# Kernel optimization log

Measured on AMD Instinct MI355X. Metric: run time of the kernel, lower is better.

Reference implementation:

```python
import jax, jax.numpy as jnp
import numpy as np

N_NODES = 50000
N_EDGES = 3200000
FEAT_IN = 2048  # pools 2:1 down to 1024


def _gcn_conv(x, row, col, W, b, n):
    # PyG GCNConv: add self-loops, symmetric D^-1/2 (A+I) D^-1/2 normalization,
    # aggregate at target (col), then bias.
    xw = x @ W  # [n, out]
    ones = jnp.ones(row.shape[0], dtype=xw.dtype)
    deg = jax.ops.segment_sum(ones, col, num_segments=n)  # includes self-loops
    dis = jax.lax.rsqrt(deg)  # deg >= 1 because of self-loops
    norm = dis[row] * dis[col]  # [E+n]
    out = jax.ops.segment_sum(norm[:, None] * xw[row], col, num_segments=n)
    return out + b


def setup_inputs() -> dict:
    key = jax.random.key(0)
    ks = jax.random.split(key, 12)
    x = jax.random.normal(ks[0], (N_NODES, FEAT_IN), dtype=jnp.float32)
    edge_index = jax.random.randint(ks[1], (2, N_EDGES), 0, N_NODES, dtype=jnp.int64)
    def lin(k, fan_in, fan_out):
        s = 1.0 / np.sqrt(fan_in)
        kw, kb = jax.random.split(k)
        W = jax.random.uniform(kw, (fan_in, fan_out), jnp.float32, -s, s)
        b = jax.random.uniform(kb, (fan_out,), jnp.float32, -s, s)
        return W, b
    w0, b0 = lin(ks[2], 1024, 512)
    w1, b1 = lin(ks[3], 512, 128)
    w2, b2 = lin(ks[4], 128, 64)
    g1_w, g1_b = lin(ks[5], 64, 32)
    g2_w, g2_b = lin(ks[6], 32, 16)
    return {
        "x": x, "edge_index": edge_index,
        "ln_w": jnp.ones((1024,), jnp.float32), "ln_b": jnp.zeros((1024,), jnp.float32),
        "w0": w0, "b0": b0, "w1": w1, "b1": b1, "w2": w2, "b2": b2,
        "g1_w": g1_w, "g1_b": g1_b, "g2_w": g2_w, "g2_b": g2_b,
    }


def reference(x, edge_index, ln_w, ln_b, w0, b0, w1, b1, w2, b2, g1_w, g1_b, g2_w, g2_b):
    n = x.shape[0]
    # AdaptiveMaxPool1d(1024): L=2048 -> exact windows of 2, stride 2
    h = x.reshape(n, 1024, 2).max(axis=-1)
    # LayerNorm(1024)
    mu = h.mean(axis=-1, keepdims=True)
    var = jnp.mean((h - mu) ** 2, axis=-1, keepdims=True)
    h = (h - mu) * jax.lax.rsqrt(var + 1e-5) * ln_w + ln_b
    # MLP with ELU (dropout is identity in eval mode)
    h = jax.nn.elu(h @ w0 + b0)
    h = jax.nn.elu(h @ w1 + b1)
    h = jax.nn.elu(h @ w2 + b2)
    # edge_index with self-loops appended (constant structure)
    sl = jnp.arange(n, dtype=edge_index.dtype)
    row = jnp.concatenate([edge_index[0], sl])
    col = jnp.concatenate([edge_index[1], sl])
    h = jax.nn.elu(_gcn_conv(h, row, col, g1_w, g1_b, n))
    return _gcn_conv(h, row, col, g2_w, g2_b, n)
```

## Files before the change

kernel.cpp:

```cpp
#include <hip/hip_runtime.h>
#include <hip/hip_bf16.h>

#define N_NODES 50000
#define N_EDGES 3200000
#define NB1 196
#define NBLK1 782
#define CAP 20480

typedef __bf16 v8bf __attribute__((ext_vector_type(8)));
typedef __bf16 v2bf __attribute__((ext_vector_type(2)));
typedef float v4f __attribute__((ext_vector_type(4)));

__device__ __forceinline__ float elu_f(float x) { return x > 0.f ? x : (expf(x) - 1.f); }

__device__ __forceinline__ float4 bf4f(ushort4 u) {
    float4 r;
    r.x = __uint_as_float(((unsigned)u.x) << 16);
    r.y = __uint_as_float(((unsigned)u.y) << 16);
    r.z = __uint_as_float(((unsigned)u.z) << 16);
    r.w = __uint_as_float(((unsigned)u.w) << 16);
    return r;
}

#define GL16(gp, lp) __builtin_amdgcn_global_load_lds( \
    (const __attribute__((address_space(1))) void*)(gp), \
    (__attribute__((address_space(3))) void*)(lp), 16, 0, 0)

__global__ void pool_ln_kernel(const float* __restrict__ x,
                               const float* __restrict__ ln_w,
                               const float* __restrict__ ln_b,
                               __bf16* __restrict__ h0,
                               const float* __restrict__ w0, const float* __restrict__ w1,
                               const float* __restrict__ w2,
                               __bf16* __restrict__ w0t, __bf16* __restrict__ w1t,
                               __bf16* __restrict__ w2t, int* __restrict__ fill196) {
    int t = threadIdx.x;
    if (blockIdx.x < 2336) {
        int idx = blockIdx.x * 256 + t;
        if (idx < NB1) fill196[idx] = idx * CAP;
        if (idx < 524288) {
            int k = idx >> 9, n = idx & 511;
            w0t[(size_t)n * 1024 + k] = (__bf16)w0[idx];
        } else if (idx < 524288 + 65536) {
            int j = idx - 524288;
            int k = j >> 7, n = j & 127;
            w1t[(size_t)n * 512 + k] = (__bf16)w1[j];
        } else if (idx < 524288 + 65536 + 8192) {
            int j = idx - 524288 - 65536;
            int k = j >> 6, n = j & 63;
            w2t[(size_t)n * 128 + k] = (__bf16)w2[j];
        }
    }
    int wave = t >> 6, lane = t & 63;
    int node = blockIdx.x * 4 + wave;
    const float4* xr = (const float4*)(x + (size_t)node * 2048);
    float4 v[8];
    #pragma unroll
    for (int j = 0; j < 8; ++j) v[j] = xr[j * 64 + lane];
    float p[16];
    float sum = 0.f, sq = 0.f;
    #pragma unroll
    for (int j = 0; j < 8; ++j) {
        p[2 * j]     = fmaxf(v[j].x, v[j].y);
        p[2 * j + 1] = fmaxf(v[j].z, v[j].w);
        sum += p[2 * j] + p[2 * j + 1];
        sq  += p[2 * j] * p[2 * j] + p[2 * j + 1] * p[2 * j + 1];
    }
    #pragma unroll
    for (int off = 32; off > 0; off >>= 1) {
        sum += __shfl_xor(sum, off);
        sq  += __shfl_xor(sq, off);
    }
    float mu = sum * (1.f / 1024.f);
    float var = sq * (1.f / 1024.f) - mu * mu;
    float rstd = rsqrtf(var + 1e-5f);
    const float2* w2p = (const float2*)ln_w;
    const float2* b2p = (const float2*)ln_b;
    #pragma unroll
    for (int j = 0; j < 8; ++j) {
        int c2 = j * 64 + lane;
        float2 w = w2p[c2], b = b2p[c2];
        v2bf o;
        o[0] = (__bf16)((p[2 * j]     - mu) * rstd * w.x + b.x);
        o[1] = (__bf16)((p[2 * j + 1] - mu) * rstd * w.y + b.y);
        *(v2bf*)(h0 + (size_t)node * 1024 + 2 * c2) = o;
    }
}

__global__ __launch_bounds__(512) void mfma_gemm0(
    const __bf16* __restrict__ A, const __bf16* __restrict__ BT,
    const float* __restrict__ bias, __bf16* __restrict__ C, int M)
{
    const int K = 1024, N = 512;
    __shared__ unsigned short lds[12288];
    const int tid = threadIdx.x;
    const int lane = tid & 63, w = tid >> 6;
    const int wr = w >> 2, wc = w & 3;
    const int m0 = blockIdx.x * 128, n0 = blockIdx.y * 256;

    int grA = m0 + (tid >> 2); if (grA > M - 1) grA = M - 1;
    const __bf16* aP = A + (size_t)grA * K + (tid & 3) * 8;
    char* ldsA = (char*)lds + tid * 16;
    const __bf16* bP0 = BT + (size_t)(n0 + (tid >> 2)) * K + (tid & 3) * 8;
    const __bf16* bP1 = BT + (size_t)(n0 + ((tid + 512) >> 2)) * K + (tid & 3) * 8;
    char* ldsB0 = (char*)lds + 8192 + tid * 16;
    char* ldsB1 = (char*)lds + 16384 + tid * 16;

    v4f acc[4][4] = {};
    const int l15 = lane & 15, l4 = lane >> 4;
    const int abase = (wr * 64 + l15) * 32 + l4 * 8;
    const int bbase = 4096 + (wc * 64 + l15) * 32 + l4 * 8;

    for (int k0 = 0; k0 < K; k0 += 32) {
        GL16(aP + k0, ldsA);
        GL16(bP0 + k0, ldsB0);
        GL16(bP1 + k0, ldsB1);
        __syncthreads();
        v8bf af[4], bfr[4];
        #pragma unroll
        for (int m = 0; m < 4; ++m) af[m]  = *(const v8bf*)&lds[abase + m * 16 * 32];
        #pragma unroll
        for (int n = 0; n < 4; ++n) bfr[n] = *(const v8bf*)&lds[bbase + n * 16 * 32];
        #pragma unroll
        for (int m = 0; m < 4; ++m)
            #pragma unroll
            for (int n = 0; n < 4; ++n)
                acc[m][n] = __builtin_amdgcn_mfma_f32_16x16x32_bf16(af[m], bfr[n], acc[m][n], 0, 0, 0);
        __syncthreads();
    }

    #pragma unroll
    for (int m = 0; m < 4; ++m) {
        #pragma unroll
        for (int j = 0; j < 4; ++j) {
            int row = m0 + wr * 64 + m * 16 + l4 * 4 + j;
            if (row >= M) continue;
            #pragma unroll
            for (int n = 0; n < 4; ++n) {
                int col = n0 + wc * 64 + n * 16 + l15;
                float v = acc[m][n][j] + bias[col];
                C[(size_t)row * N + col] = (__bf16)elu_f(v);
            }
        }
    }
}

__global__ __launch_bounds__(256) void mlp_tail_kernel(
    const __bf16* __restrict__ h1, const __bf16* __restrict__ w1t,
    const float* __restrict__ b1, const __bf16* __restrict__ w2t,
    const float* __restrict__ b2, const float* __restrict__ g1w,
    const float* __restrict__ dis, __bf16* __restrict__ xw1b, int M)
{
    extern __shared__ char smem[];
    const int G1OFF = 32768, TOFF = 40960;
    const int tid = threadIdx.x;
    const int lane = tid & 63, wave = tid >> 6;
    const int l15 = lane & 15, l4 = lane >> 4;
    const int m0 = blockIdx.x * 128;

    {
        const float4* g4 = (const float4*)g1w;
        float4* d4 = (float4*)(smem + G1OFF);
        d4[tid] = g4[tid];
        d4[tid + 256] = g4[tid + 256];
    }

    const int wr = wave >> 1, wc = wave & 1;
    const int s0 = tid, s1 = tid + 256;
    int gr0 = m0 + (s0 >> 2); if (gr0 > M - 1) gr0 = M - 1;
    int gr1 = m0 + (s1 >> 2); if (gr1 > M - 1) gr1 = M - 1;
    const __bf16* a0p = h1 + (size_t)gr0 * 512 + (s0 & 3) * 8;
    const __bf16* a1p = h1 + (size_t)gr1 * 512 + (s1 & 3) * 8;
    const __bf16* b0p = w1t + (size_t)(s0 >> 2) * 512 + (s0 & 3) * 8;
    const __bf16* b1p = w1t + (size_t)(s1 >> 2) * 512 + (s1 & 3) * 8;
    char* stA0 = smem + s0 * 16;
    char* stA1 = smem + s1 * 16;
    char* stB0 = smem + 8192 + s0 * 16;
    char* stB1 = smem + 8192 + s1 * 16;
    const int aoff = (wr * 64 + l15) * 64 + l4 * 16;
    const int boff = 8192 + (wc * 64 + l15) * 64 + l4 * 16;

    v4f acc1[4][4] = {};
    for (int k0 = 0; k0 < 512; k0 += 32) {
        GL16(a0p + k0, stA0);
        GL16(a1p + k0, stA1);
        GL16(b0p + k0, stB0);
        GL16(b1p + k0, stB1);
        __syncthreads();
        v8bf af[4], bfr[4];
        #pragma unroll
        for (int m = 0; m < 4; ++m) af[m]  = *(const v8bf*)(smem + aoff + m * 1024);
        #pragma unroll
        for (int n = 0; n < 4; ++n) bfr[n] = *(const v8bf*)(smem + boff + n * 1024);
        #pragma unroll
        for (int m = 0; m < 4; ++m)
            #pragma unroll
            for (int n = 0; n < 4; ++n)
                acc1[m][n] = __builtin_amdgcn_mfma_f32_16x16x32_bf16(af[m], bfr[n], acc1[m][n], 0, 0, 0);
        __syncthreads();
    }
    float b1c[4];
    #pragma unroll
    for (int n = 0; n < 4; ++n) b1c[n] = b1[wc * 64 + n * 16 + l15];
    #pragma unroll
    for (int m = 0; m < 4; ++m) {
        #pragma unroll
        for (int j = 0; j < 4; ++j) {
            int row = wr * 64 + m * 16 + l4 * 4 + j;
            int rx = (row & 7) << 4;
            #pragma unroll
            for (int n = 0; n < 4; ++n) {
                int colb = (wc * 64 + n * 16 + l15) * 2;
                float v = elu_f(acc1[m][n][j] + b1c[n]);
                *(__bf16*)(smem + TOFF + row * 256 + (colb ^ rx)) = (__bf16)v;
            }
        }
    }
    __syncthreads();

    const int wr2 = wave >> 1, wc2 = wave & 1;
    v4f acc2[4][2] = {};
    #pragma unroll
    for (int ks = 0; ks < 4; ++ks) {
        v8bf af2[4], bf2[2];
        #pragma unroll
        for (int m2 = 0; m2 < 4; ++m2) {
            int row = wr2 * 64 + m2 * 16 + l15;
            af2[m2] = *(const v8bf*)(smem + TOFF + row * 256 + ((ks * 64 + l4 * 16) ^ ((row & 7) << 4)));
        }
        #pragma unroll
        for (int n2 = 0; n2 < 2; ++n2) {
            int nn = wc2 * 32 + n2 * 16 + l15;
            bf2[n2] = *(const v8bf*)(w2t + nn * 128 + ks * 32 + l4 * 8);
        }
        #pragma unroll
        for (int m2 = 0; m2 < 4; ++m2)
            #pragma unroll
            for (int n2 = 0; n2 < 2; ++n2)
                acc2[m2][n2] = __builtin_amdgcn_mfma_f32_16x16x32_bf16(af2[m2], bf2[n2], acc2[m2][n2], 0, 0, 0);
    }
    __syncthreads();
    float b2c[2];
    #pragma unroll
    for (int n2 = 0; n2 < 2; ++n2) b2c[n2] = b2[wc2 * 32 + n2 * 16 + l15];
    #pragma unroll
    for (int m2 = 0; m2 < 4; ++m2) {
        #pragma unroll
        for (int j = 0; j < 4; ++j) {
            int row = wr2 * 64 + m2 * 16 + l4 * 4 + j;
            int rx = (row & 7) << 4;
            #pragma unroll
            for (int n2 = 0; n2 < 2; ++n2) {
                int col = wc2 * 32 + n2 * 16 + l15;
                float v = elu_f(acc2[m2][n2][j] + b2c[n2]);
                *(float*)(smem + row * 256 + ((col * 4) ^ rx)) = v;
            }
        }
    }
    __syncthreads();

    int r = tid >> 1;
    int nb = (tid & 1) * 16;
    int gr = m0 + r;
    float o[16] = {};
    int rx = (r & 7) << 4;
    #pragma unroll 4
    for (int k4 = 0; k4 < 16; ++k4) {
        float4 h4 = *(const float4*)(smem + r * 256 + ((k4 * 16) ^ rx));
        #pragma unroll
        for (int e = 0; e < 4; ++e) {
            const float4* gp = (const float4*)(smem + G1OFF + (k4 * 4 + e) * 128 + nb * 4);
            float hv = (e == 0) ? h4.x : (e == 1) ? h4.y : (e == 2) ? h4.z : h4.w;
            #pragma unroll
            for (int q = 0; q < 4; ++q) {
                float4 g = gp[q];
                o[4 * q + 0] += hv * g.x;
                o[4 * q + 1] += hv * g.y;
                o[4 * q + 2] += hv * g.z;
                o[4 * q + 3] += hv * g.w;
            }
        }
    }
    if (gr < M) {
        float d = dis[gr];
        v8bf pk0, pk1;
        #pragma unroll
        for (int j2 = 0; j2 < 8; ++j2) {
            pk0[j2] = (__bf16)(o[j2] * d);
            pk1[j2] = (__bf16)(o[8 + j2] * d);
        }
        *(v8bf*)(xw1b + (size_t)gr * 32 + nb) = pk0;
        *(v8bf*)(xw1b + (size_t)gr * 32 + nb + 8) = pk1;
    }
}

__global__ void p1_scatter_kernel(const int* __restrict__ row, const int* __restrict__ col,
                                  int* __restrict__ fill196, unsigned int* __restrict__ tmp) {
    __shared__ int h[NB1], bl[NB1];
    int t = threadIdx.x, b = blockIdx.x;
    if (t < NB1) h[t] = 0;
    __syncthreads();
    int base = b * 4096;
    int cc[16];
    #pragma unroll
    for (int j = 0; j < 16; ++j) {
        int e = base + j * 256 + t;
        cc[j] = (e < N_EDGES) ? col[e] : -1;
        if (cc[j] >= 0) atomicAdd(&h[cc[j] >> 8], 1);
    }
    __syncthreads();
    if (t < NB1 && h[t] > 0) bl[t] = atomicAdd(&fill196[t], h[t]);
    __syncthreads();
    #pragma unroll
    for (int j = 0; j < 16; ++j) {
        if (cc[j] >= 0) {
            int e = base + j * 256 + t;
            int pos = atomicAdd(&bl[cc[j] >> 8], 1);
            tmp[pos] = ((unsigned int)cc[j] << 16) | (unsigned int)row[e];
        }
    }
}
__global__ void p2_kernel(const unsigned int* __restrict__ tmp, const int* __restrict__ fill196,
                          int* __restrict__ csr, int* __restrict__ ptr, float* __restrict__ dis) {
    __shared__ int h2[256], b2[256], s2[256];
    __shared__ int sh_outb;
    int seg = blockIdx.x;
    int start = seg * CAP, end = fill196[seg];
    int t = threadIdx.x;
    if (t < 256) s2[t] = (t < seg) ? (fill196[t] - t * CAP) : 0;
    __syncthreads();
    for (int off = 128; off > 0; off >>= 1) {
        if (t < off) s2[t] += s2[t + off];
        __syncthreads();
    }
    if (t == 0) sh_outb = s2[0];
    if (t < 256) h2[t] = 0;
    __syncthreads();
    for (int i = start + t; i < end; i += 1024)
        atomicAdd(&h2[(tmp[i] >> 16) & 255], 1);
    __syncthreads();
    if (t < 256) s2[t] = h2[t];
    __syncthreads();
    for (int off = 1; off < 256; off <<= 1) {
        int u = 0;
        if (t < 256 && t >= off) u = s2[t - off];
        __syncthreads();
        if (t < 256) s2[t] += u;
        __syncthreads();
    }
    if (t < 256) {
        int p = sh_outb + s2[t] - h2[t];
        b2[t] = p;
        int node = (seg << 8) + t;
        if (node < N_NODES) {
            ptr[node] = p;
            dis[node] = rsqrtf((float)(h2[t] + 1));
        }
    }
    if (seg == NB1 - 1 && t == 0) ptr[N_NODES] = N_EDGES;
    __syncthreads();
    for (int i = start + t; i < end; i += 1024) {
        unsigned int v = tmp[i];
        int pos = atomicAdd(&b2[(v >> 16) & 255], 1);
        csr[pos] = (int)(v & 0xFFFFu);
    }
}

__global__ void gather1_kernel(const unsigned short* __restrict__ xw1b,
                               const int* __restrict__ csr, const int* __restrict__ ptr,
                               const float* __restrict__ dis, const float* __restrict__ g1b,
                               const float* __restrict__ g2w, __bf16* __restrict__ xw2b) {
    __shared__ float g2t[512];
    int t = threadIdx.x;
    {
        int k = t >> 4, n = t & 15;
        g2t[n * 32 + k] = g2w[t];
        int j = t + 256;
        k = j >> 4; n = j & 15;
        g2t[n * 32 + k] = g2w[j];
    }
    __syncthreads();
    int idx = blockIdx.x * 256 + t;
    int node = idx >> 3, q = idx & 7;
    if (node >= N_NODES) return;
    int s = ptr[node], e = ptr[node + 1];
    const ushort4* base = (const ushort4*)xw1b;
    float4 acc = bf4f(base[(size_t)node * 8 + q]);
    int i = s;
    for (; i + 4 <= e; i += 4) {
        float4 a = bf4f(base[(size_t)csr[i] * 8 + q]);
        float4 b = bf4f(base[(size_t)csr[i + 1] * 8 + q]);
        float4 c = bf4f(base[(size_t)csr[i + 2] * 8 + q]);
        float4 d4 = bf4f(base[(size_t)csr[i + 3] * 8 + q]);
        acc.x += (a.x + b.x) + (c.x + d4.x);
        acc.y += (a.y + b.y) + (c.y + d4.y);
        acc.z += (a.z + b.z) + (c.z + d4.z);
        acc.w += (a.w + b.w) + (c.w + d4.w);
    }
    for (; i < e; ++i) {
        float4 v = bf4f(base[(size_t)csr[i] * 8 + q]);
        acc.x += v.x; acc.y += v.y; acc.z += v.z; acc.w += v.w;
    }
    float d = dis[node];
    float4 bb = ((const float4*)g1b)[q];
    float a0 = elu_f(d * acc.x + bb.x);
    float a1 = elu_f(d * acc.y + bb.y);
    float a2 = elu_f(d * acc.z + bb.z);
    float a3 = elu_f(d * acc.w + bb.w);
    float p[16];
    const int k0 = 4 * q;
    #pragma unroll
    for (int n = 0; n < 16; ++n) {
        const float* g = &g2t[n * 32 + k0];
        p[n] = a0 * g[0] + a1 * g[1] + a2 * g[2] + a3 * g[3];
    }
    #pragma unroll
    for (int off = 1; off < 8; off <<= 1)
        #pragma unroll
        for (int n = 0; n < 16; ++n)
            p[n] += __shfl_xor(p[n], off);
    v2bf o2;
    o2[0] = (__bf16)(d * p[2 * q]);
    o2[1] = (__bf16)(d * p[2 * q + 1]);
    *(v2bf*)(xw2b + (size_t)node * 16 + 2 * q) = o2;
}

__global__ void gather2_kernel(const unsigned short* __restrict__ xw2b,
                               const int* __restrict__ csr, const int* __restrict__ ptr,
                               const float* __restrict__ dis, const float* __restrict__ g2b,
                               float* __restrict__ out) {
    int idx = blockIdx.x * 256 + threadIdx.x;
    int node = idx >> 2, q = idx & 3;
    if (node >= N_NODES) return;
    int s = ptr[node], e = ptr[node + 1];
    const ushort4* base = (const ushort4*)xw2b;
    float4 acc = bf4f(base[(size_t)node * 4 + q]);
    int i = s;
    for (; i + 4 <= e; i += 4) {
        float4 a = bf4f(base[(size_t)csr[i] * 4 + q]);
        float4 b = bf4f(base[(size_t)csr[i + 1] * 4 + q]);
        float4 c = bf4f(base[(size_t)csr[i + 2] * 4 + q]);
        float4 d4 = bf4f(base[(size_t)csr[i + 3] * 4 + q]);
        acc.x += (a.x + b.x) + (c.x + d4.x);
        acc.y += (a.y + b.y) + (c.y + d4.y);
        acc.z += (a.z + b.z) + (c.z + d4.z);
        acc.w += (a.w + b.w) + (c.w + d4.w);
    }
    for (; i < e; ++i) {
        float4 v = bf4f(base[(size_t)csr[i] * 4 + q]);
        acc.x += v.x; acc.y += v.y; acc.z += v.z; acc.w += v.w;
    }
    float d = dis[node];
    float4 bb = ((const float4*)g2b)[q];
    float4 o;
    o.x = d * acc.x + bb.x; o.y = d * acc.y + bb.y;
    o.z = d * acc.z + bb.z; o.w = d * acc.w + bb.w;
    ((float4*)out)[idx] = o;
}

extern "C" void kernel_launch(void* const* d_in, const int* in_sizes, int n_in,
                              void* d_out, int out_size, void* d_ws, size_t ws_size,
                              hipStream_t stream) {
    const float* x    = (const float*)d_in[0];
    const int*   ei   = (const int*)d_in[1];
    const int*   row  = ei;
    const int*   col  = ei + N_EDGES;
    const float* ln_w = (const float*)d_in[2];
    const float* ln_b = (const float*)d_in[3];
    const float* w0   = (const float*)d_in[4];
    const float* b0   = (const float*)d_in[5];
    const float* w1   = (const float*)d_in[6];
    const float* b1   = (const float*)d_in[7];
    const float* w2   = (const float*)d_in[8];
    const float* b2   = (const float*)d_in[9];
    const float* g1w  = (const float*)d_in[10];
    const float* g1b  = (const float*)d_in[11];
    const float* g2w  = (const float*)d_in[12];
    const float* g2b  = (const float*)d_in[13];
    float* out = (float*)d_out;

    char* W = (char*)d_ws;
    __bf16* h0   = (__bf16*)(W + 0);
    __bf16* h1   = (__bf16*)(W + 102400000);
    float*  dis  = (float*) (W + 179200000);
    __bf16* xw1b = (__bf16*)(W + 179400192);
    __bf16* xw2b = (__bf16*)(W + 185800192);
    __bf16* w0t  = (__bf16*)(W + 195400192);
    __bf16* w1t  = (__bf16*)(W + 196448768);
    __bf16* w2t  = (__bf16*)(W + 196579840);
    int*    csr  = (int*)(W + 200000000);
    int*    ptr  = (int*)(W + 213000192);
    unsigned int* tmp = (unsigned int*)(W + 214000128);
    int*    fill196 = (int*)(W + 231000064);

    pool_ln_kernel<<<N_NODES / 4, 256, 0, stream>>>(
        x, ln_w, ln_b, h0, w0, w1, w2, w0t, w1t, w2t, fill196);

    {
        dim3 g((N_NODES + 127) / 128, 2);
        mfma_gemm0<<<g, 512, 0, stream>>>(h0, w0t, b0, h1, N_NODES);
    }

    p1_scatter_kernel<<<NBLK1, 256, 0, stream>>>(row, col, fill196, tmp);
    p2_kernel<<<NB1, 1024, 0, stream>>>(tmp, fill196, csr, ptr, dis);

    mlp_tail_kernel<<<(N_NODES + 127) / 128, 256, 73728, stream>>>(
        h1, w1t, b1, w2t, b2, g1w, dis, xw1b, N_NODES);

    gather1_kernel<<<((N_NODES * 8) + 255) / 256, 256, 0, stream>>>(
        (const unsigned short*)xw1b, csr, ptr, dis, g1b, g2w, xw2b);

    gather2_kernel<<<((N_NODES * 4) + 255) / 256, 256, 0, stream>>>(
        (const unsigned short*)xw2b, csr, ptr, dis, g2b, out);
}
```

Measured before the change: 376.7 us.

## Fuse edge bucketing into pool/LN and CSR build into GEMM0 launch

```diff
diff --git a/kernel.cpp b/kernel.cpp
--- a/kernel.cpp
+++ b/kernel.cpp
@@ -6,6 +6,8 @@
 #define NB1 196
 #define NBLK1 782
 #define CAP 20480
+#define WT_BLKS 2336
+#define G0_BLKS 782
 
 typedef __bf16 v8bf __attribute__((ext_vector_type(8)));
 typedef __bf16 v2bf __attribute__((ext_vector_type(2)));
@@ -33,11 +35,49 @@
                                const float* __restrict__ w0, const float* __restrict__ w1,
                                const float* __restrict__ w2,
                                __bf16* __restrict__ w0t, __bf16* __restrict__ w1t,
-                               __bf16* __restrict__ w2t, int* __restrict__ fill196) {
+                               __bf16* __restrict__ w2t, int* __restrict__ fill196,
+                               const int* __restrict__ erow, const int* __restrict__ ecol,
+                               unsigned int* __restrict__ tmp) {
+    __shared__ int h[NB1], bl[NB1];
     int t = threadIdx.x;
-    if (blockIdx.x < 2336) {
+    {
+        int wave = t >> 6, lane = t & 63;
+        int node = blockIdx.x * 4 + wave;
+        const float4* xr = (const float4*)(x + (size_t)node * 2048);
+        float4 v[8];
+        #pragma unroll
+        for (int j = 0; j < 8; ++j) v[j] = xr[j * 64 + lane];
+        float p[16];
+        float sum = 0.f, sq = 0.f;
+        #pragma unroll
+        for (int j = 0; j < 8; ++j) {
+            p[2 * j]     = fmaxf(v[j].x, v[j].y);
+            p[2 * j + 1] = fmaxf(v[j].z, v[j].w);
+            sum += p[2 * j] + p[2 * j + 1];
+            sq  += p[2 * j] * p[2 * j] + p[2 * j + 1] * p[2 * j + 1];
+        }
+        #pragma unroll
+        for (int off = 32; off > 0; off >>= 1) {
+            sum += __shfl_xor(sum, off);
+            sq  += __shfl_xor(sq, off);
+        }
+        float mu = sum * (1.f / 1024.f);
+        float var = sq * (1.f / 1024.f) - mu * mu;
+        float rstd = rsqrtf(var + 1e-5f);
+        const float2* w2p = (const float2*)ln_w;
+        const float2* b2p = (const float2*)ln_b;
+        #pragma unroll
+        for (int j = 0; j < 8; ++j) {
+            int c2 = j * 64 + lane;
+            float2 w = w2p[c2], b = b2p[c2];
+            v2bf o;
+            o[0] = (__bf16)((p[2 * j]     - mu) * rstd * w.x + b.x);
+            o[1] = (__bf16)((p[2 * j + 1] - mu) * rstd * w.y + b.y);
+            *(v2bf*)(h0 + (size_t)node * 1024 + 2 * c2) = o;
+        }
+    }
+    if (blockIdx.x < WT_BLKS) {
         int idx = blockIdx.x * 256 + t;
-        if (idx < NB1) fill196[idx] = idx * CAP;
         if (idx < 524288) {
             int k = idx >> 9, n = idx & 511;
             w0t[(size_t)n * 1024 + k] = (__bf16)w0[idx];
@@ -50,53 +90,104 @@
             int k = j >> 6, n = j & 63;
             w2t[(size_t)n * 128 + k] = (__bf16)w2[j];
         }
-    }
-    int wave = t >> 6, lane = t & 63;
-    int node = blockIdx.x * 4 + wave;
-    const float4* xr = (const float4*)(x + (size_t)node * 2048);
-    float4 v[8];
-    #pragma unroll
-    for (int j = 0; j < 8; ++j) v[j] = xr[j * 64 + lane];
-    float p[16];
-    float sum = 0.f, sq = 0.f;
-    #pragma unroll
-    for (int j = 0; j < 8; ++j) {
-        p[2 * j]     = fmaxf(v[j].x, v[j].y);
-        p[2 * j + 1] = fmaxf(v[j].z, v[j].w);
-        sum += p[2 * j] + p[2 * j + 1];
-        sq  += p[2 * j] * p[2 * j] + p[2 * j + 1] * p[2 * j + 1];
-    }
-    #pragma unroll
-    for (int off = 32; off > 0; off >>= 1) {
-        sum += __shfl_xor(sum, off);
-        sq  += __shfl_xor(sq, off);
-    }
-    float mu = sum * (1.f / 1024.f);
-    float var = sq * (1.f / 1024.f) - mu * mu;
-    float rstd = rsqrtf(var + 1e-5f);
-    const float2* w2p = (const float2*)ln_w;
-    const float2* b2p = (const float2*)ln_b;
-    #pragma unroll
-    for (int j = 0; j < 8; ++j) {
-        int c2 = j * 64 + lane;
-        float2 w = w2p[c2], b = b2p[c2];
-        v2bf o;
-        o[0] = (__bf16)((p[2 * j]     - mu) * rstd * w.x + b.x);
-        o[1] = (__bf16)((p[2 * j + 1] - mu) * rstd * w.y + b.y);
-        *(v2bf*)(h0 + (size_t)node * 1024 + 2 * c2) = o;
-    }
-}
-
-__global__ __launch_bounds__(512) void mfma_gemm0(
+    } else if (blockIdx.x < WT_BLKS + NBLK1) {
+        int cb = blockIdx.x - WT_BLKS;
+        if (t < NB1) h[t] = 0;
+        __syncthreads();
+        int base = cb * 4096;
+        int cc[16];
+        #pragma unroll
+        for (int j = 0; j < 16; ++j) {
+            int e = base + j * 256 + t;
+            cc[j] = (e < N_EDGES) ? ecol[e] : -1;
+            if (cc[j] >= 0) atomicAdd(&h[cc[j] >> 8], 1);
+        }
+        __syncthreads();
+        if (t < NB1 && h[t] > 0)
+            bl[t] = t * CAP + atomicAdd(&fill196[t], h[t]);
+        __syncthreads();
+        #pragma unroll
+        for (int j = 0; j < 16; ++j) {
+            if (cc[j] >= 0) {
+                int e = base + j * 256 + t;
+                int pos = atomicAdd(&bl[cc[j] >> 8], 1);
+                tmp[pos] = ((unsigned int)cc[j] << 16) | (unsigned int)erow[e];
+            }
+        }
+    }
+}
+
+__global__ __launch_bounds__(512) void gemm0_p2_kernel(
     const __bf16* __restrict__ A, const __bf16* __restrict__ BT,
-    const float* __restrict__ bias, __bf16* __restrict__ C, int M)
+    const float* __restrict__ bias, __bf16* __restrict__ C, int M,
+    const unsigned int* __restrict__ tmp, const int* __restrict__ fill196,
+    int* __restrict__ csr, int* __restrict__ ptr, float* __restrict__ dis)
 {
+    __shared__ char smem[24576];
+    const int tid = threadIdx.x;
+    int b = blockIdx.x;
+
+    if (b >= G0_BLKS) {
+        int seg = b - G0_BLKS;
+        int* h2 = (int*)smem;
+        int* b2 = (int*)smem + 256;
+        int* s2 = (int*)smem + 512;
+        int* shp = (int*)smem + 768;
+        int start = seg * CAP;
+        int cnt = fill196[seg];
+        int end = start + cnt;
+        int t = tid;
+        if (t < 256) s2[t] = (t < seg) ? fill196[t] : 0;
+        __syncthreads();
+        for (int off = 128; off > 0; off >>= 1) {
+            if (t < off) s2[t] += s2[t + off];
+            __syncthreads();
+        }
+        if (t == 0) shp[0] = s2[0];
+        if (t < 256) h2[t] = 0;
+        __syncthreads();
+        for (int i = start + t; i < end; i += 512)
+            atomicAdd(&h2[(tmp[i] >> 16) & 255], 1);
+        __syncthreads();
+        if (t < 256) s2[t] = h2[t];
+        __syncthreads();
+        for (int off = 1; off < 256; off <<= 1) {
+            int u = 0;
+            if (t < 256 && t >= off) u = s2[t - off];
+            __syncthreads();
+            if (t < 256) s2[t] += u;
+            __syncthreads();
+        }
+        if (t < 256) {
+            int p = shp[0] + s2[t] - h2[t];
+            b2[t] = p;
+            int node = (seg << 8) + t;
+            if (node < N_NODES) {
+                ptr[node] = p;
+                dis[node] = rsqrtf((float)(h2[t] + 1));
+            }
+        }
+        if (seg == NB1 - 1 && t == 0) ptr[N_NODES] = N_EDGES;
+        __syncthreads();
+        for (int i = start + t; i < end; i += 512) {
+            unsigned int v = tmp[i];
+            int pos = atomicAdd(&b2[(v >> 16) & 255], 1);
+            csr[pos] = (int)(v & 0xFFFFu);
+        }
+        return;
+    }
+
+    {
+        const int q = 97, r = 6;
+        int xcd = b & 7, pos = b >> 3;
+        int wg = (xcd < r ? xcd * (q + 1) : r * (q + 1) + (xcd - r) * q) + pos;
+        b = wg;
+    }
     const int K = 1024, N = 512;
-    __shared__ unsigned short lds[12288];
-    const int tid = threadIdx.x;
+    unsigned short* lds = (unsigned short*)smem;
     const int lane = tid & 63, w = tid >> 6;
     const int wr = w >> 2, wc = w & 3;
-    const int m0 = blockIdx.x * 128, n0 = blockIdx.y * 256;
+    const int m0 = (b >> 1) * 128, n0 = (b & 1) * 256;
 
     int grA = m0 + (tid >> 2); if (grA > M - 1) grA = M - 1;
     const __bf16* aP = A + (size_t)grA * K + (tid & 3) * 8;
@@ -291,78 +382,6 @@
         }
         *(v8bf*)(xw1b + (size_t)gr * 32 + nb) = pk0;
         *(v8bf*)(xw1b + (size_t)gr * 32 + nb + 8) = pk1;
-    }
-}
-
-__global__ void p1_scatter_kernel(const int* __restrict__ row, const int* __restrict__ col,
-                                  int* __restrict__ fill196, unsigned int* __restrict__ tmp) {
-    __shared__ int h[NB1], bl[NB1];
-    int t = threadIdx.x, b = blockIdx.x;
-    if (t < NB1) h[t] = 0;
-    __syncthreads();
-    int base = b * 4096;
-    int cc[16];
-    #pragma unroll
-    for (int j = 0; j < 16; ++j) {
-        int e = base + j * 256 + t;
-        cc[j] = (e < N_EDGES) ? col[e] : -1;
-        if (cc[j] >= 0) atomicAdd(&h[cc[j] >> 8], 1);
-    }
-    __syncthreads();
-    if (t < NB1 && h[t] > 0) bl[t] = atomicAdd(&fill196[t], h[t]);
-    __syncthreads();
-    #pragma unroll
-    for (int j = 0; j < 16; ++j) {
-        if (cc[j] >= 0) {
-            int e = base + j * 256 + t;
-            int pos = atomicAdd(&bl[cc[j] >> 8], 1);
-            tmp[pos] = ((unsigned int)cc[j] << 16) | (unsigned int)row[e];
-        }
-    }
-}
-__global__ void p2_kernel(const unsigned int* __restrict__ tmp, const int* __restrict__ fill196,
-                          int* __restrict__ csr, int* __restrict__ ptr, float* __restrict__ dis) {
-    __shared__ int h2[256], b2[256], s2[256];
-    __shared__ int sh_outb;
-    int seg = blockIdx.x;
-    int start = seg * CAP, end = fill196[seg];
-    int t = threadIdx.x;
-    if (t < 256) s2[t] = (t < seg) ? (fill196[t] - t * CAP) : 0;
-    __syncthreads();
-    for (int off = 128; off > 0; off >>= 1) {
-        if (t < off) s2[t] += s2[t + off];
-        __syncthreads();
-    }
-    if (t == 0) sh_outb = s2[0];
-    if (t < 256) h2[t] = 0;
-    __syncthreads();
-    for (int i = start + t; i < end; i += 1024)
-        atomicAdd(&h2[(tmp[i] >> 16) & 255], 1);
-    __syncthreads();
-    if (t < 256) s2[t] = h2[t];
-    __syncthreads();
-    for (int off = 1; off < 256; off <<= 1) {
-        int u = 0;
-        if (t < 256 && t >= off) u = s2[t - off];
-        __syncthreads();
-        if (t < 256) s2[t] += u;
-        __syncthreads();
-    }
-    if (t < 256) {
-        int p = sh_outb + s2[t] - h2[t];
-        b2[t] = p;
-        int node = (seg << 8) + t;
-        if (node < N_NODES) {
-            ptr[node] = p;
-            dis[node] = rsqrtf((float)(h2[t] + 1));
-        }
-    }
-    if (seg == NB1 - 1 && t == 0) ptr[N_NODES] = N_EDGES;
-    __syncthreads();
-    for (int i = start + t; i < end; i += 1024) {
-        unsigned int v = tmp[i];
-        int pos = atomicAdd(&b2[(v >> 16) & 255], 1);
-        csr[pos] = (int)(v & 0xFFFFu);
     }
 }
 
@@ -493,16 +512,13 @@
     unsigned int* tmp = (unsigned int*)(W + 214000128);
     int*    fill196 = (int*)(W + 231000064);
 
+    hipMemsetAsync(fill196, 0, NB1 * sizeof(int), stream);
+
     pool_ln_kernel<<<N_NODES / 4, 256, 0, stream>>>(
-        x, ln_w, ln_b, h0, w0, w1, w2, w0t, w1t, w2t, fill196);
-
-    {
-        dim3 g((N_NODES + 127) / 128, 2);
-        mfma_gemm0<<<g, 512, 0, stream>>>(h0, w0t, b0, h1, N_NODES);
-    }
-
-    p1_scatter_kernel<<<NBLK1, 256, 0, stream>>>(row, col, fill196, tmp);
-    p2_kernel<<<NB1, 1024, 0, stream>>>(tmp, fill196, csr, ptr, dis);
+        x, ln_w, ln_b, h0, w0, w1, w2, w0t, w1t, w2t, fill196, row, col, tmp);
+
+    gemm0_p2_kernel<<<G0_BLKS + NB1, 512, 0, stream>>>(
+        h0, w0t, b0, h1, N_NODES, tmp, fill196, csr, ptr, dis);
 
     mlp_tail_kernel<<<(N_NODES + 127) / 128, 256, 73728, stream>>>(
         h1, w1t, b1, w2t, b2, g1w, dis, xw1b, N_NODES);
```

After: 356.3 us. -5.4%, faster.
